# Performance work log

Measured on AMD Instinct MI355X. Metric: run time of the kernel, lower is better.

## Reference

```python
import jax, jax.numpy as jnp
import numpy as np

GUMBEL_BETA = 0.0036  # gumbel_beta init kwarg
N1, N2, BOX_DIM = 160, 1024, 256


def _center_sigmoid_offsets(data):
    # CenterSigmoidBoxTensor: softplus with beta=10, then sigmoid
    sp = jax.nn.softplus(10.0 * data[..., 1, :]) / 10.0
    zmin = jax.nn.sigmoid(data[..., 0, :] - sp)
    zmax = jax.nn.sigmoid(data[..., 0, :] + sp)
    return zmin, zmax


def setup_inputs() -> dict:
    key = jax.random.key(0)
    k1, k2 = jax.random.split(key)
    box1s = jax.random.normal(k1, (N1, 2, BOX_DIM), dtype=jnp.float32)
    box2s = jax.random.normal(k2, (N2, 2, BOX_DIM), dtype=jnp.float32)
    return {"box1s": box1s, "box2s": box2s}


def reference(box1s, box2s):
    gb = GUMBEL_BETA
    z1, Z1 = _center_sigmoid_offsets(box1s)  # [N1, D]
    z2, Z2 = _center_sigmoid_offsets(box2s)  # [N2, D]

    # Pairwise: i over box2s (outer), j over box1s (inner) -> [N2, N1, D]
    a, b = z2[:, None, :], z1[None, :, :]
    # gb * logsumexp([a/gb, b/gb], 0) == max(a,b) + gb*log1p(exp(-|a-b|/gb))
    lse_min = jnp.maximum(a, b) + gb * jnp.log1p(jnp.exp(-jnp.abs(a - b) / gb))
    inter_min = jnp.maximum(lse_min, jnp.maximum(a, b))

    A, B = Z2[:, None, :], Z1[None, :, :]
    # -gb * logsumexp([-A/gb, -B/gb], 0) == min(A,B) - gb*log1p(exp(-|A-B|/gb))
    lse_max = jnp.minimum(A, B) - gb * jnp.log1p(jnp.exp(-jnp.abs(A - B) / gb))
    inter_max = jnp.minimum(lse_max, jnp.minimum(A, B))

    n2, n1, d = inter_min.shape
    return inter_min.reshape(n2 * n1, d), inter_max.reshape(n2 * n1, d)
```

## Files before the change

kernel.cpp:

```cpp
#include <hip/hip_runtime.h>
#include <hip/hip_bf16.h>

#define BN1 160
#define BN2 1024
#define BD  256

#define GB_F     0.0036f
#define INV_GB_F (1.0f / 0.0036f)

__device__ float g_z1min[BN1 * BD];
__device__ float g_z1max[BN1 * BD];
__device__ float g_z2min[BN2 * BD];
__device__ float g_z2max[BN2 * BD];

__device__ __forceinline__ float softplus10(float x) {
    float y = 10.0f * x;
    float t = __expf(-fabsf(y));
    return (fmaxf(y, 0.0f) + __logf(1.0f + t)) * 0.1f;
}

__device__ __forceinline__ float sigmoidf(float x) {
    return 1.0f / (1.0f + __expf(-x));
}

__global__ __launch_bounds__(256) void precompute_kernel(
        const float* __restrict__ box1s, const float* __restrict__ box2s) {
    int idx = blockIdx.x * 256 + threadIdx.x;
    if (idx < BN2 * BD) {
        int n = idx >> 8;
        int d = idx & (BD - 1);
        float c  = box2s[n * 2 * BD + d];
        float sp = softplus10(box2s[n * 2 * BD + BD + d]);
        g_z2min[idx] = sigmoidf(c - sp);
        g_z2max[idx] = sigmoidf(c + sp);
    } else {
        int j = idx - BN2 * BD;
        if (j < BN1 * BD) {
            int n = j >> 8;
            int d = j & (BD - 1);
            float c  = box1s[n * 2 * BD + d];
            float sp = softplus10(box1s[n * 2 * BD + BD + d]);
            g_z1min[j] = sigmoidf(c - sp);
            g_z1max[j] = sigmoidf(c + sp);
        }
    }
}

union F4 {
    float4 v;
    float f[4];
};

__global__ __launch_bounds__(256) void pairs_kernel(float* __restrict__ out) {
    const int t    = threadIdx.x;
    const int row  = blockIdx.x * 4 + (t >> 6);
    const int d0   = (t & 63) << 2;

    const int i2 = row / BN1;
    const int i1 = row - i2 * BN1;

    F4 a, A, b, B;
    a.v = *(const float4*)(g_z2min + i2 * BD + d0);
    A.v = *(const float4*)(g_z2max + i2 * BD + d0);
    b.v = *(const float4*)(g_z1min + i1 * BD + d0);
    B.v = *(const float4*)(g_z1max + i1 * BD + d0);

    F4 o0, o1;
#pragma unroll
    for (int j = 0; j < 4; ++j) {
        float av = a.f[j], bv = b.f[j];
        float m  = fmaxf(av, bv);
        float c0 = GB_F * __logf(1.0f + __expf(-fabsf(av - bv) * INV_GB_F));
        o0.f[j]  = fmaxf(m + c0, m);

        float Av = A.f[j], Bv = B.f[j];
        float M  = fminf(Av, Bv);
        float c1 = GB_F * __logf(1.0f + __expf(-fabsf(Av - Bv) * INV_GB_F));
        o1.f[j]  = fminf(M - c1, M);
    }

    const size_t base = (size_t)row * BD + d0;
    const size_t half = (size_t)BN2 * BN1 * BD;
    *(float4*)(out + base)        = o0.v;
    *(float4*)(out + half + base) = o1.v;
}

extern "C" void kernel_launch(void* const* d_in, const int* in_sizes, int n_in,
                              void* d_out, int out_size, void* d_ws, size_t ws_size,
                              hipStream_t stream) {
    const float* box1s = (const float*)d_in[0];
    const float* box2s = (const float*)d_in[1];
    float* out = (float*)d_out;

    precompute_kernel<<<1184, 256, 0, stream>>>(box1s, box2s);

    pairs_kernel<<<(BN2 * BN1) / 4, 256, 0, stream>>>(out);
}
```

Measured before the change: 328.1 us.

## Process two box1 rows per thread with nontemporal stores and raw exp2/log2

Each thread now computes two output rows that share the same box2 vectors, which halves the block count and reuses the a/A loads. Output writes use nontemporal stores so the large write-only result bypasses cache retention. The softplus-style correction switches to the hardware exp2/log2 builtins with constants folded for base-2 conversion. This trades some per-thread register pressure and a small change in floating-point rounding for fewer instructions and less cache pollution.

```diff
diff --git a/kernel.cpp b/kernel.cpp
--- a/kernel.cpp
+++ b/kernel.cpp
@@ -1,12 +1,16 @@
 #include <hip/hip_runtime.h>
-#include <hip/hip_bf16.h>
 
 #define BN1 160
 #define BN2 1024
 #define BD  256
 
-#define GB_F     0.0036f
-#define INV_GB_F (1.0f / 0.0036f)
+#define GB_LN2 0.0024953256f
+#define K2     400.74862f
+
+typedef float f32x4 __attribute__((ext_vector_type(4)));
+
+#define EXP2F(x) __builtin_amdgcn_exp2f(x)
+#define LOG2F(x) __builtin_amdgcn_logf(x)
 
 __device__ float g_z1min[BN1 * BD];
 __device__ float g_z1max[BN1 * BD];
@@ -47,42 +51,53 @@
 }
 
 union F4 {
-    float4 v;
+    f32x4 v;
     float f[4];
 };
 
+__device__ __forceinline__ float gumbel_min(float x, float y) {
+    float m = fmaxf(x, y);
+    float c = GB_LN2 * LOG2F(1.0f + EXP2F(-fabsf(x - y) * K2));
+    return fmaxf(m + c, m);
+}
+
+__device__ __forceinline__ float gumbel_max(float x, float y) {
+    float m = fminf(x, y);
+    float c = GB_LN2 * LOG2F(1.0f + EXP2F(-fabsf(x - y) * K2));
+    return fminf(m - c, m);
+}
+
 __global__ __launch_bounds__(256) void pairs_kernel(float* __restrict__ out) {
-    const int t    = threadIdx.x;
-    const int row  = blockIdx.x * 4 + (t >> 6);
-    const int d0   = (t & 63) << 2;
+    const int t   = threadIdx.x;
+    const int bid = blockIdx.x;
+    const int i2  = bid / 20;
+    const int i1  = (bid - i2 * 20) * 8 + ((t >> 6) << 1);
+    const int d0  = (t & 63) << 2;
 
-    const int i2 = row / BN1;
-    const int i1 = row - i2 * BN1;
+    F4 a, A, b0, B0, b1, B1;
+    a.v  = *(const f32x4*)(g_z2min + i2 * BD + d0);
+    A.v  = *(const f32x4*)(g_z2max + i2 * BD + d0);
+    b0.v = *(const f32x4*)(g_z1min + i1 * BD + d0);
+    B0.v = *(const f32x4*)(g_z1max + i1 * BD + d0);
+    b1.v = *(const f32x4*)(g_z1min + (i1 + 1) * BD + d0);
+    B1.v = *(const f32x4*)(g_z1max + (i1 + 1) * BD + d0);
 
-    F4 a, A, b, B;
-    a.v = *(const float4*)(g_z2min + i2 * BD + d0);
-    A.v = *(const float4*)(g_z2max + i2 * BD + d0);
-    b.v = *(const float4*)(g_z1min + i1 * BD + d0);
-    B.v = *(const float4*)(g_z1max + i1 * BD + d0);
-
-    F4 o0, o1;
+    F4 o00, o01, o10, o11;
 #pragma unroll
     for (int j = 0; j < 4; ++j) {
-        float av = a.f[j], bv = b.f[j];
-        float m  = fmaxf(av, bv);
-        float c0 = GB_F * __logf(1.0f + __expf(-fabsf(av - bv) * INV_GB_F));
-        o0.f[j]  = fmaxf(m + c0, m);
-
-        float Av = A.f[j], Bv = B.f[j];
-        float M  = fminf(Av, Bv);
-        float c1 = GB_F * __logf(1.0f + __expf(-fabsf(Av - Bv) * INV_GB_F));
-        o1.f[j]  = fminf(M - c1, M);
+        const float av = a.f[j], Av = A.f[j];
+        o00.f[j] = gumbel_min(av, b0.f[j]);
+        o01.f[j] = gumbel_max(Av, B0.f[j]);
+        o10.f[j] = gumbel_min(av, b1.f[j]);
+        o11.f[j] = gumbel_max(Av, B1.f[j]);
     }
 
-    const size_t base = (size_t)row * BD + d0;
     const size_t half = (size_t)BN2 * BN1 * BD;
-    *(float4*)(out + base)        = o0.v;
-    *(float4*)(out + half + base) = o1.v;
+    const size_t base = (size_t)(i2 * BN1 + i1) * BD + d0;
+    __builtin_nontemporal_store(o00.v, (f32x4*)(out + base));
+    __builtin_nontemporal_store(o10.v, (f32x4*)(out + base + BD));
+    __builtin_nontemporal_store(o01.v, (f32x4*)(out + half + base));
+    __builtin_nontemporal_store(o11.v, (f32x4*)(out + half + base + BD));
 }
 
 extern "C" void kernel_launch(void* const* d_in, const int* in_sizes, int n_in,
@@ -94,5 +109,5 @@
 
     precompute_kernel<<<1184, 256, 0, stream>>>(box1s, box2s);
 
-    pairs_kernel<<<(BN2 * BN1) / 4, 256, 0, stream>>>(out);
+    pairs_kernel<<<BN2 * (BN1 / 8), 256, 0, stream>>>(out);
 }
```

Result: no change. 332.4 us (+1.3%).
